# Kernel optimization log

Hardware: AMD Instinct MI355X
Metric: run time of the kernel (lower is better)

## Reference

```python
import jax, jax.numpy as jnp
import numpy as np
from jax import lax

EXPANDED_BASE_DIM = 256
VISUAL_FEATURE_DIM = 768
HIDDEN_DIM = 1024
INPUT_DIM = EXPANDED_BASE_DIM + VISUAL_FEATURE_DIM
B, K = 256, 128


def setup_inputs() -> dict:
    key = jax.random.key(0)
    k1, k2, k3, k4, k5, k6 = jax.random.split(key, 6)
    s = 1.0 / np.sqrt(HIDDEN_DIM)  # PyTorch GRU init scale
    return {
        "base_expanded_seq": jax.random.normal(k1, (B, K, EXPANDED_BASE_DIM), jnp.float32),
        "visual_seq": jax.random.normal(k2, (B, K, VISUAL_FEATURE_DIM), jnp.float32),
        # PyTorch layout: gates stacked as [r, z, n] along first axis (3H)
        "W_ih": jax.random.uniform(k3, (3 * HIDDEN_DIM, INPUT_DIM), jnp.float32, -s, s),
        "W_hh": jax.random.uniform(k4, (3 * HIDDEN_DIM, HIDDEN_DIM), jnp.float32, -s, s),
        "b_ih": jax.random.uniform(k5, (3 * HIDDEN_DIM,), jnp.float32, -s, s),
        "b_hh": jax.random.uniform(k6, (3 * HIDDEN_DIM,), jnp.float32, -s, s),
    }


def reference(base_expanded_seq, visual_seq, W_ih, W_hh, b_ih, b_hh):
    # Faithful to GRUEncoder.forward: per-step concat -> GRU cell, return final h.
    x_seq = jnp.concatenate([base_expanded_seq, visual_seq], axis=-1)  # (B,K,I)
    Bb, Kk, _ = x_seq.shape
    H = W_hh.shape[1]
    # Precompute input projections for all steps (same math, batched GEMM)
    x_proj = jnp.einsum('bki,gi->bkg', x_seq, W_ih) + b_ih  # (B,K,3H)
    x_proj_t = jnp.swapaxes(x_proj, 0, 1)  # (K,B,3H)

    def step(h, xp):
        hp = h @ W_hh.T + b_hh  # (B,3H)
        xr, xz, xn = jnp.split(xp, 3, axis=-1)
        hr, hz, hn = jnp.split(hp, 3, axis=-1)
        r = jax.nn.sigmoid(xr + hr)
        z = jax.nn.sigmoid(xz + hz)
        n = jnp.tanh(xn + r * hn)
        h_new = (1.0 - z) * n + z * h
        return h_new, None

    h0 = jnp.zeros((Bb, H), x_seq.dtype)
    h_final, _ = lax.scan(step, h0, x_proj_t)
    return h_final  # (B, H) == h[-1] for num_layers=1
```

## Files before the change

### kernel.cpp

```cpp
#include <hip/hip_runtime.h>

#define BATCH 256
#define SEQ   128
#define IDIM  1024
#define HDIM  1024
#define G3    3072
#define RS    100

typedef __attribute__((ext_vector_type(8))) short bf16x8;
typedef __attribute__((ext_vector_type(4))) short s16x4;
typedef __attribute__((ext_vector_type(4))) float f32x4;

__device__ __forceinline__ short f2bf(float f) {
    union { float f; unsigned u; } x; x.f = f;
    unsigned r = x.u + 0x7fffu + ((x.u >> 16) & 1u);
    return (short)(r >> 16);
}
__device__ __forceinline__ float bf2f(unsigned short u) {
    union { unsigned u; float f; } x; x.u = ((unsigned)u) << 16;
    return x.f;
}

__device__ __forceinline__ void st_llc_b64(short* p, s16x4 v) {
    asm volatile("global_store_dwordx2 %0, %1, off sc0 sc1" :: "v"(p), "v"(v) : "memory");
}
__device__ __forceinline__ void st_llc_b32(unsigned* p, unsigned v) {
    asm volatile("global_store_dword %0, %1, off sc0 sc1" :: "v"(p), "v"(v) : "memory");
}
#define LDH(dst, p, OFF) \
    asm volatile("global_load_dwordx4 %0, %1, off offset:" OFF " sc0 sc1" \
                 : "=v"(dst) : "v"(p))
#define LDX(dst, p) \
    asm volatile("global_load_dwordx2 %0, %1, off" : "=v"(dst) : "v"(p))

__global__ void cvt_w(const float* __restrict__ wih, const float* __restrict__ whh,
                      short* __restrict__ wihb, short* __restrict__ whhb) {
    int i = blockIdx.x * 256 + threadIdx.x;
    const float* s; short* d; int j;
    if (i < 786432) { s = wih; d = wihb; j = i; }
    else            { s = whh; d = whhb; j = i - 786432; }
    const float4 v = *((const float4*)s + j);
    s16x4 o;
    o[0] = f2bf(v.x); o[1] = f2bf(v.y); o[2] = f2bf(v.z); o[3] = f2bf(v.w);
    *(s16x4*)(d + (size_t)j * 4) = o;
}

__global__ __launch_bounds__(256, 2) void gemm_xproj(
    const float* __restrict__ base, const float* __restrict__ vis,
    const short* __restrict__ wihb, const float* __restrict__ bih,
    short* __restrict__ xp)
{
    __shared__ union {
        struct { short A[2][128 * 64]; short B[2][128 * 64]; } ab;
        short C[128 * 136];
    } sm;
    const int tid = threadIdx.x;
    const int bid = blockIdx.x;
    const int nt = bid % 24, mt = bid / 24;
    const int m0 = mt * 128, n0 = nt * 128;
    const int lane = tid & 63, w = tid >> 6;
    const int wm = w >> 1, wn = w & 1;
    const int l15 = lane & 15, quad = lane >> 4;

    f32x4 acc[4][4];
#pragma unroll
    for (int i = 0; i < 4; ++i)
#pragma unroll
        for (int j = 0; j < 4; ++j) acc[i][j] = (f32x4){0.f, 0.f, 0.f, 0.f};

    const int arow = tid >> 3;
    const int acol8 = (tid & 7) * 8;

    float4 pv0[4], pv1[4];

    auto issueA = [&](int kt) {
        const int col = kt * 64 + acol8;
#pragma unroll
        for (int is = 0; is < 4; ++is) {
            const int row = m0 + is * 32 + arow;
            const float* s = (col < 256)
                ? (base + (size_t)row * 256 + col)
                : (vis  + (size_t)row * 768 + (col - 256));
            pv0[is] = *(const float4*)s;
            pv1[is] = *(const float4*)(s + 4);
        }
    };
    auto stage = [&](int buf, int kt) {
        const int k0 = kt * 64;
#pragma unroll
        for (int is = 0; is < 4; ++is) {
            union { unsigned u[4]; bf16x8 v; } pk;
            asm("v_cvt_pk_bf16_f32 %0, %1, %2" : "=v"(pk.u[0]) : "v"(pv0[is].x), "v"(pv0[is].y));
            asm("v_cvt_pk_bf16_f32 %0, %1, %2" : "=v"(pk.u[1]) : "v"(pv0[is].z), "v"(pv0[is].w));
            asm("v_cvt_pk_bf16_f32 %0, %1, %2" : "=v"(pk.u[2]) : "v"(pv1[is].x), "v"(pv1[is].y));
            asm("v_cvt_pk_bf16_f32 %0, %1, %2" : "=v"(pk.u[3]) : "v"(pv1[is].z), "v"(pv1[is].w));
            *(bf16x8*)&sm.ab.A[buf][is * 2048 + tid * 8] = pk.v;
            __builtin_amdgcn_global_load_lds(
                (const __attribute__((address_space(1))) void*)(wihb + (size_t)(n0 + is * 32 + arow) * 1024 + k0 + acol8),
                (__attribute__((address_space(3))) void*)&sm.ab.B[buf][is * 2048 + tid * 8],
                16, 0, 0);
        }
    };

    issueA(0);
    stage(0, 0);
    issueA(1);
    __syncthreads();

    for (int kt = 0; kt < 16; ++kt) {
        const int cur = kt & 1, nxt = cur ^ 1;
        if (kt < 15) {
            stage(nxt, kt + 1);
            if (kt < 14) issueA(kt + 2);
        }
#pragma unroll
        for (int s2 = 0; s2 < 2; ++s2) {
            bf16x8 af[4], bfv[4];
#pragma unroll
            for (int i = 0; i < 4; ++i)
                af[i] = *(const bf16x8*)&sm.ab.A[cur][(wm * 64 + i * 16 + l15) * 64 + s2 * 32 + quad * 8];
#pragma unroll
            for (int j = 0; j < 4; ++j)
                bfv[j] = *(const bf16x8*)&sm.ab.B[cur][(wn * 64 + j * 16 + l15) * 64 + s2 * 32 + quad * 8];
#pragma unroll
            for (int i = 0; i < 4; ++i)
#pragma unroll
                for (int j = 0; j < 4; ++j)
                    acc[i][j] = __builtin_amdgcn_mfma_f32_16x16x32_bf16(af[i], bfv[j], acc[i][j], 0, 0, 0);
        }
        __syncthreads();
    }
#pragma unroll
    for (int j = 0; j < 4; ++j) {
        const int cn = wn * 64 + j * 16 + l15;
        const float bv = bih[n0 + cn];
#pragma unroll
        for (int i = 0; i < 4; ++i) {
            const int rb = wm * 64 + i * 16 + quad * 4;
#pragma unroll
            for (int r = 0; r < 4; ++r)
                sm.C[(rb + r) * 136 + cn] = f2bf(acc[i][j][r] + bv);
        }
    }
    __syncthreads();
    {
        const int row = tid >> 1, c0 = (tid & 1) * 64;
        const int gm = m0 + row;
        short* dst = xp + ((size_t)(gm & 127) * 256 + (size_t)(gm >> 7)) * 3072 + n0 + c0;
        const short* src = &sm.C[row * 136 + c0];
#pragma unroll
        for (int c = 0; c < 64; c += 8)
            *(bf16x8*)(dst + c) = *(const bf16x8*)(src + c);
    }
}

__global__ __launch_bounds__(256, 1) void gru_rec(
    const short* __restrict__ xp, const short* __restrict__ whhb,
    const float* __restrict__ bhh, short* __restrict__ hbuf,
    float* __restrict__ out, unsigned* __restrict__ flags)
{
    __shared__ float red[128 * RS];
    const int tid = threadIdx.x;
    const int bid = blockIdx.x;
    const int bt = bid >> 5;
    const int ct = bid & 31;
    const int lane = tid & 63, w = tid >> 6;
    const int l15 = lane & 15, quad = lane >> 4;
    const int bm0 = bt * 32;
    const int kbase = w * 256 + quad * 8;

    bf16x8 Bf[6][8];
#pragma unroll
    for (int g = 0; g < 6; ++g) {
        const size_t col = (size_t)((g >> 1) * 1024 + ct * 32 + (g & 1) * 16 + l15);
#pragma unroll
        for (int kk = 0; kk < 8; ++kk)
            Bf[g][kk] = *(const bf16x8*)(whhb + col * 1024 + kbase + kk * 32);
    }

    const int er = tid >> 3;
    const int ec0 = (tid & 7) * 4;
    const f32x4 bhr = *(const f32x4*)(bhh + ct * 32 + ec0);
    const f32x4 bhz = *(const f32x4*)(bhh + 1024 + ct * 32 + ec0);
    const f32x4 bhn = *(const f32x4*)(bhh + 2048 + ct * 32 + ec0);

    unsigned* const myflag = flags + bt * 32 + ct;
    const unsigned* const pollp = flags + bt * 32 + (lane & 31);

    float hold[4] = {0.f, 0.f, 0.f, 0.f};
    s16x4 xc[3], xn_[3];
    {
        const size_t rb = (size_t)(bm0 + er) * 3072 + ct * 32 + ec0;
#pragma unroll
        for (int g = 0; g < 3; ++g) xc[g] = *(const s16x4*)(xp + rb + g * 1024);
    }

    for (int step = 0; step < 128; ++step) {
        if (step > 0) {
            const unsigned tgt = (unsigned)step;
            unsigned fv;
            do {
                asm volatile("global_load_dword %0, %1, off sc0 sc1" : "=v"(fv) : "v"(pollp));
                asm volatile("s_waitcnt vmcnt(0)" : "+v"(fv) :: "memory");
            } while (__ballot(fv < tgt));
        }
        const short* hr_ = hbuf + (size_t)(step & 1) * (256 * 1024);
        short* hw_ = hbuf + (size_t)((step + 1) & 1) * (256 * 1024);

        bf16x8 A0[8], A1[8];
        const short* p0 = hr_ + (size_t)(bm0 + l15) * 1024 + kbase;
        const short* p1 = p0 + 16 * 1024;
        LDH(A0[0], p0, "0");   LDH(A0[1], p0, "64");  LDH(A0[2], p0, "128"); LDH(A0[3], p0, "192");
        LDH(A0[4], p0, "256"); LDH(A0[5], p0, "320"); LDH(A0[6], p0, "384"); LDH(A0[7], p0, "448");
        LDH(A1[0], p1, "0");   LDH(A1[1], p1, "64");  LDH(A1[2], p1, "128"); LDH(A1[3], p1, "192");
        LDH(A1[4], p1, "256"); LDH(A1[5], p1, "320"); LDH(A1[6], p1, "384"); LDH(A1[7], p1, "448");
        asm volatile("s_waitcnt vmcnt(0)"
            : "+v"(A0[0]), "+v"(A0[1]), "+v"(A0[2]), "+v"(A0[3]),
              "+v"(A0[4]), "+v"(A0[5]), "+v"(A0[6]), "+v"(A0[7]),
              "+v"(A1[0]), "+v"(A1[1]), "+v"(A1[2]), "+v"(A1[3]),
              "+v"(A1[4]), "+v"(A1[5]), "+v"(A1[6]), "+v"(A1[7])
            :: "memory");
        if (step < 127) {
            const short* rb = xp + ((size_t)(step + 1) * 256 + bm0 + er) * 3072 + ct * 32 + ec0;
            LDX(xn_[0], rb); LDX(xn_[1], rb + 1024); LDX(xn_[2], rb + 2048);
        }

        f32x4 acc[2][6];
#pragma unroll
        for (int i = 0; i < 2; ++i)
#pragma unroll
            for (int g = 0; g < 6; ++g) acc[i][g] = (f32x4){0.f, 0.f, 0.f, 0.f};
#pragma unroll
        for (int kk = 0; kk < 8; ++kk) {
#pragma unroll
            for (int g = 0; g < 6; ++g) {
                acc[0][g] = __builtin_amdgcn_mfma_f32_16x16x32_bf16(A0[kk], Bf[g][kk], acc[0][g], 0, 0, 0);
                acc[1][g] = __builtin_amdgcn_mfma_f32_16x16x32_bf16(A1[kk], Bf[g][kk], acc[1][g], 0, 0, 0);
            }
        }
#pragma unroll
        for (int i = 0; i < 2; ++i)
#pragma unroll
            for (int g = 0; g < 6; ++g) {
                const int c96 = (g >> 1) * 32 + (g & 1) * 16 + l15;
                const int rb = w * 32 + i * 16 + quad * 4;
#pragma unroll
                for (int r = 0; r < 4; ++r)
                    red[(rb + r) * RS + c96] = acc[i][g][r];
            }
        __syncthreads();
        f32x4 sr = bhr, sz = bhz, sn = bhn;
#pragma unroll
        for (int ww = 0; ww < 4; ++ww) {
            const float* rbp = &red[(ww * 32 + er) * RS];
            sr += *(const f32x4*)(rbp + ec0);
            sz += *(const f32x4*)(rbp + 32 + ec0);
            sn += *(const f32x4*)(rbp + 64 + ec0);
        }
        s16x4 hpk;
#pragma unroll
        for (int i = 0; i < 4; ++i) {
            const float xr = bf2f((unsigned short)xc[0][i]);
            const float xz = bf2f((unsigned short)xc[1][i]);
            const float xnv = bf2f((unsigned short)xc[2][i]);
            const float rg = 1.f / (1.f + __expf(-(xr + sr[i])));
            const float zg = 1.f / (1.f + __expf(-(xz + sz[i])));
            const float e2 = __expf(2.f * (xnv + rg * sn[i]));
            const float ng = 1.f - 2.f / (e2 + 1.f);
            const float hv = (1.f - zg) * ng + zg * hold[i];
            hold[i] = hv;
            hpk[i] = f2bf(hv);
        }
        if (step < 127) {
            st_llc_b64(&hw_[(size_t)(bm0 + er) * 1024 + ct * 32 + ec0], hpk);
            asm volatile("s_waitcnt vmcnt(0)"
                : "+v"(xn_[0]), "+v"(xn_[1]), "+v"(xn_[2]) :: "memory");
            __syncthreads();
            if (tid == 0) st_llc_b32(myflag, (unsigned)(step + 1));
            xc[0] = xn_[0]; xc[1] = xn_[1]; xc[2] = xn_[2];
        } else {
            __syncthreads();
        }
    }
    float4 o4; o4.x = hold[0]; o4.y = hold[1]; o4.z = hold[2]; o4.w = hold[3];
    *(float4*)(out + (size_t)(bm0 + er) * 1024 + ct * 32 + ec0) = o4;
}

extern "C" void kernel_launch(void* const* d_in, const int* in_sizes, int n_in,
                              void* d_out, int out_size, void* d_ws, size_t ws_size,
                              hipStream_t stream) {
    (void)in_sizes; (void)n_in; (void)out_size; (void)ws_size;
    const float* base = (const float*)d_in[0];
    const float* vis  = (const float*)d_in[1];
    const float* wih  = (const float*)d_in[2];
    const float* whh  = (const float*)d_in[3];
    const float* bih  = (const float*)d_in[4];
    const float* bhh  = (const float*)d_in[5];

    char* ws = (char*)d_ws;
    short*    xp   = (short*)(ws + 0);
    short*    wihb = (short*)(ws + 201326592);
    short*    whhb = (short*)(ws + 207618048);
    short*    hbuf = (short*)(ws + 213909504);
    unsigned* flg  = (unsigned*)(ws + 214958080);

    hipMemsetAsync(hbuf, 0, 1048576, stream);
    hipMemsetAsync(flg, 0, 4096, stream);

    cvt_w<<<dim3(6144), dim3(256), 0, stream>>>(wih, whh, wihb, whhb);
    gemm_xproj<<<dim3(6144), dim3(256), 0, stream>>>(base, vis, wihb, bih, xp);
    gru_rec<<<dim3(256), dim3(256), 0, stream>>>(xp, whhb, bhh, hbuf, (float*)d_out, flg);
}
```

Measured before the change: 1.192 ms.

## Validate hidden-state reads with per-chunk tags instead of store-fence before flag

Each block now writes an XOR tag (step counter mixed with the packed h values) next to every h chunk in a double-buffered tag array. It no longer waits for its h stores to complete and for a block barrier before publishing its flag. Readers still poll the flags, then load h together with the matching tags and retry until every tag agrees with the data and the step. This removes the store-completion wait from the per-step critical path, at the cost of extra tag loads and stores, a possible retry loop, and a small chance that an XOR checksum matches on stale data.

```diff
diff --git a/kernel.cpp b/kernel.cpp
--- a/kernel.cpp
+++ b/kernel.cpp
@@ -28,6 +28,9 @@
     asm volatile("global_store_dword %0, %1, off sc0 sc1" :: "v"(p), "v"(v) : "memory");
 }
 #define LDH(dst, p, OFF) \
+    asm volatile("global_load_dwordx4 %0, %1, off offset:" OFF " sc0 sc1" \
+                 : "=v"(dst) : "v"(p))
+#define LDT(dst, p, OFF) \
     asm volatile("global_load_dwordx4 %0, %1, off offset:" OFF " sc0 sc1" \
                  : "=v"(dst) : "v"(p))
 #define LDX(dst, p) \
@@ -157,7 +160,8 @@
 __global__ __launch_bounds__(256, 1) void gru_rec(
     const short* __restrict__ xp, const short* __restrict__ whhb,
     const float* __restrict__ bhh, short* __restrict__ hbuf,
-    float* __restrict__ out, unsigned* __restrict__ flags)
+    float* __restrict__ out, unsigned* __restrict__ flags,
+    unsigned* __restrict__ tags)
 {
     __shared__ float red[128 * RS];
     const int tid = threadIdx.x;
@@ -187,8 +191,14 @@
     unsigned* const myflag = flags + bt * 32 + ct;
     const unsigned* const pollp = flags + bt * 32 + (lane & 31);
 
+    const int pcol = ct * 32 + ec0;
+    const int tagoff = (bm0 + er) * 256 + (pcol >> 8) * 64
+                     + ((((pcol >> 3) & 3) * 2 + ((pcol >> 2) & 1)) * 8)
+                     + ((pcol >> 5) & 7);
+
     float hold[4] = {0.f, 0.f, 0.f, 0.f};
     s16x4 xc[3], xn_[3];
+    xn_[0] = (s16x4){0,0,0,0}; xn_[1] = (s16x4){0,0,0,0}; xn_[2] = (s16x4){0,0,0,0};
     {
         const size_t rb = (size_t)(bm0 + er) * 3072 + ct * 32 + ec0;
 #pragma unroll
@@ -206,20 +216,41 @@
         }
         const short* hr_ = hbuf + (size_t)(step & 1) * (256 * 1024);
         short* hw_ = hbuf + (size_t)((step + 1) & 1) * (256 * 1024);
+        const unsigned* tr_ = tags + (size_t)(step & 1) * 65536;
+        unsigned* tw_ = tags + (size_t)((step + 1) & 1) * 65536;
 
         bf16x8 A0[8], A1[8];
+        uint4 T0a, T0b, T0c, T0d, T1a, T1b, T1c, T1d;
         const short* p0 = hr_ + (size_t)(bm0 + l15) * 1024 + kbase;
         const short* p1 = p0 + 16 * 1024;
-        LDH(A0[0], p0, "0");   LDH(A0[1], p0, "64");  LDH(A0[2], p0, "128"); LDH(A0[3], p0, "192");
-        LDH(A0[4], p0, "256"); LDH(A0[5], p0, "320"); LDH(A0[6], p0, "384"); LDH(A0[7], p0, "448");
-        LDH(A1[0], p1, "0");   LDH(A1[1], p1, "64");  LDH(A1[2], p1, "128"); LDH(A1[3], p1, "192");
-        LDH(A1[4], p1, "256"); LDH(A1[5], p1, "320"); LDH(A1[6], p1, "384"); LDH(A1[7], p1, "448");
-        asm volatile("s_waitcnt vmcnt(0)"
-            : "+v"(A0[0]), "+v"(A0[1]), "+v"(A0[2]), "+v"(A0[3]),
-              "+v"(A0[4]), "+v"(A0[5]), "+v"(A0[6]), "+v"(A0[7]),
-              "+v"(A1[0]), "+v"(A1[1]), "+v"(A1[2]), "+v"(A1[3]),
-              "+v"(A1[4]), "+v"(A1[5]), "+v"(A1[6]), "+v"(A1[7])
-            :: "memory");
+        const unsigned* tq0 = tr_ + (size_t)(bm0 + l15) * 256 + w * 64 + quad * 16;
+        const unsigned* tq1 = tq0 + 16 * 256;
+        const unsigned stepu = (unsigned)step;
+        for (;;) {
+            LDH(A0[0], p0, "0");   LDH(A0[1], p0, "64");  LDH(A0[2], p0, "128"); LDH(A0[3], p0, "192");
+            LDH(A0[4], p0, "256"); LDH(A0[5], p0, "320"); LDH(A0[6], p0, "384"); LDH(A0[7], p0, "448");
+            LDH(A1[0], p1, "0");   LDH(A1[1], p1, "64");  LDH(A1[2], p1, "128"); LDH(A1[3], p1, "192");
+            LDH(A1[4], p1, "256"); LDH(A1[5], p1, "320"); LDH(A1[6], p1, "384"); LDH(A1[7], p1, "448");
+            LDT(T0a, tq0, "0"); LDT(T0b, tq0, "16"); LDT(T0c, tq0, "32"); LDT(T0d, tq0, "48");
+            LDT(T1a, tq1, "0"); LDT(T1b, tq1, "16"); LDT(T1c, tq1, "32"); LDT(T1d, tq1, "48");
+            asm volatile("s_waitcnt vmcnt(0)" ::: "memory");
+            __builtin_amdgcn_sched_barrier(0);
+            unsigned bad = 0;
+#define CK(A, TJ0, TJ1, C) do { union { bf16x8 v; uint4 u; } _a; _a.v = (A); \
+            bad |= ((TJ0).C ^ stepu ^ _a.u.x ^ _a.u.y); \
+            bad |= ((TJ1).C ^ stepu ^ _a.u.z ^ _a.u.w); } while (0)
+            CK(A0[0], T0a, T0c, x); CK(A0[1], T0a, T0c, y);
+            CK(A0[2], T0a, T0c, z); CK(A0[3], T0a, T0c, w);
+            CK(A0[4], T0b, T0d, x); CK(A0[5], T0b, T0d, y);
+            CK(A0[6], T0b, T0d, z); CK(A0[7], T0b, T0d, w);
+            CK(A1[0], T1a, T1c, x); CK(A1[1], T1a, T1c, y);
+            CK(A1[2], T1a, T1c, z); CK(A1[3], T1a, T1c, w);
+            CK(A1[4], T1b, T1d, x); CK(A1[5], T1b, T1d, y);
+            CK(A1[6], T1b, T1d, z); CK(A1[7], T1b, T1d, w);
+#undef CK
+            if (__ballot(bad != 0) == 0) break;
+        }
+        if (step > 0) { xc[0] = xn_[0]; xc[1] = xn_[1]; xc[2] = xn_[2]; }
         if (step < 127) {
             const short* rb = xp + ((size_t)(step + 1) * 256 + bm0 + er) * 3072 + ct * 32 + ec0;
             LDX(xn_[0], rb); LDX(xn_[1], rb + 1024); LDX(xn_[2], rb + 2048);
@@ -257,6 +288,7 @@
             sz += *(const f32x4*)(rbp + 32 + ec0);
             sn += *(const f32x4*)(rbp + 64 + ec0);
         }
+        __syncthreads();
         s16x4 hpk;
 #pragma unroll
         for (int i = 0; i < 4; ++i) {
@@ -272,14 +304,10 @@
             hpk[i] = f2bf(hv);
         }
         if (step < 127) {
+            union { s16x4 v; unsigned u[2]; } hp; hp.v = hpk;
             st_llc_b64(&hw_[(size_t)(bm0 + er) * 1024 + ct * 32 + ec0], hpk);
-            asm volatile("s_waitcnt vmcnt(0)"
-                : "+v"(xn_[0]), "+v"(xn_[1]), "+v"(xn_[2]) :: "memory");
-            __syncthreads();
+            st_llc_b32(tw_ + tagoff, (unsigned)(step + 1) ^ hp.u[0] ^ hp.u[1]);
             if (tid == 0) st_llc_b32(myflag, (unsigned)(step + 1));
-            xc[0] = xn_[0]; xc[1] = xn_[1]; xc[2] = xn_[2];
-        } else {
-            __syncthreads();
         }
     }
     float4 o4; o4.x = hold[0]; o4.y = hold[1]; o4.z = hold[2]; o4.w = hold[3];
@@ -304,10 +332,12 @@
     short*    hbuf = (short*)(ws + 213909504);
     unsigned* flg  = (unsigned*)(ws + 214958080);
 
-    hipMemsetAsync(hbuf, 0, 1048576, stream);
-    hipMemsetAsync(flg, 0, 4096, stream);
+    (void)hipMemsetAsync(hbuf, 0, 1048576, stream);
+    (void)hipMemsetAsync(flg, 0, 4096, stream);
 
     cvt_w<<<dim3(6144), dim3(256), 0, stream>>>(wih, whh, wihb, whhb);
     gemm_xproj<<<dim3(6144), dim3(256), 0, stream>>>(base, vis, wihb, bih, xp);
-    gru_rec<<<dim3(256), dim3(256), 0, stream>>>(xp, whhb, bhh, hbuf, (float*)d_out, flg);
-}
+    (void)hipMemsetAsync(wihb, 0, 524288, stream);
+    gru_rec<<<dim3(256), dim3(256), 0, stream>>>(xp, whhb, bhh, hbuf, (float*)d_out, flg,
+                                                 (unsigned*)wihb);
+}
```

Result: slower. 1.336 ms (+12.1%).

## Replace flag-based h handoff with self-validating tagged packets in global memory

Applied to the files above, without the earlier changes.

The hidden state exchange now writes 16-byte packets containing two bf16 pairs plus an XOR tag encoding the step. Readers spin on the data itself and validate the tags instead of relying only on a release/acquire flag ordering. This aims to cut the store-wait-barrier-flag latency on the critical path of each recurrence step. In exchange it doubles the traffic of the h reads, still polls the flags, and reuses the W_ih bf16 workspace as the mirror buffer after the GEMM. That reuse needs an extra memset, and the tag check can in principle alias when the data happens to match the tag pattern.

```diff
diff --git a/kernel.cpp b/kernel.cpp
--- a/kernel.cpp
+++ b/kernel.cpp
@@ -10,6 +10,7 @@
 typedef __attribute__((ext_vector_type(8))) short bf16x8;
 typedef __attribute__((ext_vector_type(4))) short s16x4;
 typedef __attribute__((ext_vector_type(4))) float f32x4;
+typedef __attribute__((ext_vector_type(4))) unsigned u32x4;
 
 __device__ __forceinline__ short f2bf(float f) {
     union { float f; unsigned u; } x; x.f = f;
@@ -21,13 +22,7 @@
     return x.f;
 }
 
-__device__ __forceinline__ void st_llc_b64(short* p, s16x4 v) {
-    asm volatile("global_store_dwordx2 %0, %1, off sc0 sc1" :: "v"(p), "v"(v) : "memory");
-}
-__device__ __forceinline__ void st_llc_b32(unsigned* p, unsigned v) {
-    asm volatile("global_store_dword %0, %1, off sc0 sc1" :: "v"(p), "v"(v) : "memory");
-}
-#define LDH(dst, p, OFF) \
+#define LDG(dst, p, OFF) \
     asm volatile("global_load_dwordx4 %0, %1, off offset:" OFF " sc0 sc1" \
                  : "=v"(dst) : "v"(p))
 #define LDX(dst, p) \
@@ -156,7 +151,7 @@
 
 __global__ __launch_bounds__(256, 1) void gru_rec(
     const short* __restrict__ xp, const short* __restrict__ whhb,
-    const float* __restrict__ bhh, short* __restrict__ hbuf,
+    const float* __restrict__ bhh, unsigned* __restrict__ hmir,
     float* __restrict__ out, unsigned* __restrict__ flags)
 {
     __shared__ float red[128 * RS];
@@ -189,6 +184,7 @@
 
     float hold[4] = {0.f, 0.f, 0.f, 0.f};
     s16x4 xc[3], xn_[3];
+    xn_[0] = (s16x4){0,0,0,0}; xn_[1] = (s16x4){0,0,0,0}; xn_[2] = (s16x4){0,0,0,0};
     {
         const size_t rb = (size_t)(bm0 + er) * 3072 + ct * 32 + ec0;
 #pragma unroll
@@ -204,22 +200,49 @@
                 asm volatile("s_waitcnt vmcnt(0)" : "+v"(fv) :: "memory");
             } while (__ballot(fv < tgt));
         }
-        const short* hr_ = hbuf + (size_t)(step & 1) * (256 * 1024);
-        short* hw_ = hbuf + (size_t)((step + 1) & 1) * (256 * 1024);
-
+        const unsigned* mr_ = hmir + (size_t)(step & 1) * 262144;
+        unsigned* mw_ = hmir + (size_t)((step + 1) & 1) * 262144;
+
+        u32x4 Ga[16], Gb[16];
+        const unsigned* g0 = mr_ + ((size_t)(bm0 + l15) * 256 + w * 64 + quad * 2) * 4;
+        const unsigned* g1 = g0 + 16 * 256 * 4;
+        const unsigned stepu = (unsigned)step;
+        for (;;) {
+            LDG(Ga[0],  g0, "0");   LDG(Ga[1],  g0, "16");
+            LDG(Ga[2],  g0, "128"); LDG(Ga[3],  g0, "144");
+            LDG(Ga[4],  g0, "256"); LDG(Ga[5],  g0, "272");
+            LDG(Ga[6],  g0, "384"); LDG(Ga[7],  g0, "400");
+            LDG(Ga[8],  g0, "512"); LDG(Ga[9],  g0, "528");
+            LDG(Ga[10], g0, "640"); LDG(Ga[11], g0, "656");
+            LDG(Ga[12], g0, "768"); LDG(Ga[13], g0, "784");
+            LDG(Ga[14], g0, "896"); LDG(Ga[15], g0, "912");
+            LDG(Gb[0],  g1, "0");   LDG(Gb[1],  g1, "16");
+            LDG(Gb[2],  g1, "128"); LDG(Gb[3],  g1, "144");
+            LDG(Gb[4],  g1, "256"); LDG(Gb[5],  g1, "272");
+            LDG(Gb[6],  g1, "384"); LDG(Gb[7],  g1, "400");
+            LDG(Gb[8],  g1, "512"); LDG(Gb[9],  g1, "528");
+            LDG(Gb[10], g1, "640"); LDG(Gb[11], g1, "656");
+            LDG(Gb[12], g1, "768"); LDG(Gb[13], g1, "784");
+            LDG(Gb[14], g1, "896"); LDG(Gb[15], g1, "912");
+            asm volatile("s_waitcnt vmcnt(0)" ::: "memory");
+            __builtin_amdgcn_sched_barrier(0);
+            unsigned bad = 0;
+#pragma unroll
+            for (int j = 0; j < 16; ++j) {
+                bad |= (Ga[j][2] ^ stepu ^ Ga[j][0] ^ Ga[j][1]);
+                bad |= (Gb[j][2] ^ stepu ^ Gb[j][0] ^ Gb[j][1]);
+            }
+            if (__ballot(bad != 0) == 0) break;
+        }
         bf16x8 A0[8], A1[8];
-        const short* p0 = hr_ + (size_t)(bm0 + l15) * 1024 + kbase;
-        const short* p1 = p0 + 16 * 1024;
-        LDH(A0[0], p0, "0");   LDH(A0[1], p0, "64");  LDH(A0[2], p0, "128"); LDH(A0[3], p0, "192");
-        LDH(A0[4], p0, "256"); LDH(A0[5], p0, "320"); LDH(A0[6], p0, "384"); LDH(A0[7], p0, "448");
-        LDH(A1[0], p1, "0");   LDH(A1[1], p1, "64");  LDH(A1[2], p1, "128"); LDH(A1[3], p1, "192");
-        LDH(A1[4], p1, "256"); LDH(A1[5], p1, "320"); LDH(A1[6], p1, "384"); LDH(A1[7], p1, "448");
-        asm volatile("s_waitcnt vmcnt(0)"
-            : "+v"(A0[0]), "+v"(A0[1]), "+v"(A0[2]), "+v"(A0[3]),
-              "+v"(A0[4]), "+v"(A0[5]), "+v"(A0[6]), "+v"(A0[7]),
-              "+v"(A1[0]), "+v"(A1[1]), "+v"(A1[2]), "+v"(A1[3]),
-              "+v"(A1[4]), "+v"(A1[5]), "+v"(A1[6]), "+v"(A1[7])
-            :: "memory");
+#pragma unroll
+        for (int kk = 0; kk < 8; ++kk) {
+            union { u32x4 u; bf16x8 v; } t0, t1;
+            t0.u = (u32x4){Ga[2 * kk][0], Ga[2 * kk][1], Ga[2 * kk + 1][0], Ga[2 * kk + 1][1]};
+            t1.u = (u32x4){Gb[2 * kk][0], Gb[2 * kk][1], Gb[2 * kk + 1][0], Gb[2 * kk + 1][1]};
+            A0[kk] = t0.v; A1[kk] = t1.v;
+        }
+        if (step > 0) { xc[0] = xn_[0]; xc[1] = xn_[1]; xc[2] = xn_[2]; }
         if (step < 127) {
             const short* rb = xp + ((size_t)(step + 1) * 256 + bm0 + er) * 3072 + ct * 32 + ec0;
             LDX(xn_[0], rb); LDX(xn_[1], rb + 1024); LDX(xn_[2], rb + 2048);
@@ -257,6 +280,7 @@
             sz += *(const f32x4*)(rbp + 32 + ec0);
             sn += *(const f32x4*)(rbp + 64 + ec0);
         }
+        __syncthreads();
         s16x4 hpk;
 #pragma unroll
         for (int i = 0; i < 4; ++i) {
@@ -272,14 +296,16 @@
             hpk[i] = f2bf(hv);
         }
         if (step < 127) {
-            st_llc_b64(&hw_[(size_t)(bm0 + er) * 1024 + ct * 32 + ec0], hpk);
-            asm volatile("s_waitcnt vmcnt(0)"
-                : "+v"(xn_[0]), "+v"(xn_[1]), "+v"(xn_[2]) :: "memory");
-            __syncthreads();
-            if (tid == 0) st_llc_b32(myflag, (unsigned)(step + 1));
-            xc[0] = xn_[0]; xc[1] = xn_[1]; xc[2] = xn_[2];
-        } else {
-            __syncthreads();
+            union { s16x4 v; unsigned u[2]; } hp; hp.v = hpk;
+            const unsigned tag = (unsigned)(step + 1) ^ hp.u[0] ^ hp.u[1];
+            u32x4 pkt; pkt[0] = hp.u[0]; pkt[1] = hp.u[1]; pkt[2] = tag; pkt[3] = tag;
+            unsigned* gp = mw_ + ((size_t)(bm0 + er) * 256 + ct * 8 + (tid & 7)) * 4;
+            asm volatile("global_store_dwordx4 %0, %1, off sc0 sc1" :: "v"(gp), "v"(pkt) : "memory");
+            __builtin_amdgcn_s_barrier();
+            if (tid == 0) {
+                const unsigned sv = (unsigned)(step + 1);
+                asm volatile("global_store_dword %0, %1, off sc0 sc1" :: "v"(myflag), "v"(sv) : "memory");
+            }
         }
     }
     float4 o4; o4.x = hold[0]; o4.y = hold[1]; o4.z = hold[2]; o4.w = hold[3];
@@ -301,13 +327,13 @@
     short*    xp   = (short*)(ws + 0);
     short*    wihb = (short*)(ws + 201326592);
     short*    whhb = (short*)(ws + 207618048);
-    short*    hbuf = (short*)(ws + 213909504);
     unsigned* flg  = (unsigned*)(ws + 214958080);
 
-    hipMemsetAsync(hbuf, 0, 1048576, stream);
-    hipMemsetAsync(flg, 0, 4096, stream);
+    (void)hipMemsetAsync(flg, 0, 4096, stream);
 
     cvt_w<<<dim3(6144), dim3(256), 0, stream>>>(wih, whh, wihb, whhb);
     gemm_xproj<<<dim3(6144), dim3(256), 0, stream>>>(base, vis, wihb, bih, xp);
-    gru_rec<<<dim3(256), dim3(256), 0, stream>>>(xp, whhb, bhh, hbuf, (float*)d_out, flg);
-}
+    (void)hipMemsetAsync(wihb, 0, 2097152, stream);
+    gru_rec<<<dim3(256), dim3(256), 0, stream>>>(xp, whhb, bhh, (unsigned*)wihb,
+                                                 (float*)d_out, flg);
+}
```

New measurement: 1.410 ms. +18.3%, slower.
